# Optimization experiments

Hardware: AMD Instinct MI355X
Metric: run time of the kernel (lower is better)

## Reference

```python
import jax, jax.numpy as jnp
import numpy as np

PI = 3.14159265359  # TFPI constant from the source


def expected_relu(mu, sigma_sq):
    # Expected ReLU of N(mu, sigma_sq); exact ReLU where sigma_sq == 0 (observed).
    missing = sigma_sq != 0.0
    imputed = jnp.where(missing, sigma_sq, 1e-20)
    s = jnp.sqrt(imputed)
    w = mu / s
    vals = s * (jnp.exp(-0.5 * w * w) / jnp.sqrt(2.0 * PI)
                + 0.5 * w * (1.0 + jax.scipy.special.erf(w / jnp.sqrt(2.0))))
    return jnp.where(missing, vals, 0.5 * (mu + jnp.abs(mu)))


def setup_inputs() -> dict:
    key = jax.random.key(0)
    k0, k1, k2, k3, k4 = jax.random.split(key, 5)
    N, P, C, U = 65536, 256, 3, 512
    x = jax.random.normal(k0, (N, P), dtype=jnp.float32)
    nan_mask = jax.random.bernoulli(k1, 0.15, (N, P))
    x = jnp.where(nan_mask, jnp.nan, x)
    component_means = 0.5 * jax.random.normal(k2, (P, C), dtype=jnp.float32)
    component_vars = jax.random.uniform(k3, (P, C), dtype=jnp.float32, minval=0.5, maxval=1.5)
    component_logits = jnp.ones((C,), dtype=jnp.float32)
    kernel = jax.random.normal(k4, (P, U), dtype=jnp.float32) / np.float32(np.sqrt(P))
    bias = jnp.zeros((U,), dtype=jnp.float32)
    return {"x": x, "component_means": component_means, "component_vars": component_vars,
            "component_logits": component_logits, "kernel": kernel, "bias": bias}


def reference(x, component_means, component_vars, component_logits, kernel, bias):
    # x: [N, P] with NaNs; component_means/vars: [P, C]; logits: [C]; kernel: [P, U]; bias: [U]
    nan_mask = jnp.isnan(x)                       # [N, P]
    x_safe = jnp.where(nan_mask, 0.0, x)          # NaN-free copy (masked out below)
    mu_t = component_means.T                      # [C, P]
    var_t = component_vars.T                      # [C, P]
    # mvn_loglikelihood with NaN entries contributing 0
    q = -jnp.square(x_safe[:, None, :] - mu_t) / var_t / 2.0 - jnp.log(2.0 * PI * var_t) / 2.0  # [N, C, P]
    q = jnp.where(nan_mask[:, None, :], 0.0, q)
    loglik = jnp.sum(q, axis=-1)                  # [N, C]
    reweighted_p = jax.nn.softmax(component_logits + loglik, axis=-1)  # [N, C]
    # Impute missing entries with component means; variance nonzero only where missing
    means = jnp.where(nan_mask[..., None], component_means, x_safe[..., None])   # [N, P, C]
    variances = jnp.where(nan_mask[..., None], component_vars, 0.0)              # [N, P, C]
    layer_mean = jnp.einsum('npc,pu->cnu', means, kernel) + bias                 # [C, N, U]
    layer_var = jnp.einsum('npc,pu->cnu', variances, jnp.square(kernel))         # [C, N, U]
    layer_activation = expected_relu(layer_mean, layer_var)                      # [C, N, U]
    return jnp.einsum('nc,cnu->nu', reweighted_p, layer_activation)              # [N, U]
```

## Files before the change

### kernel.cpp

```cpp
#include <hip/hip_runtime.h>
#include <hip/hip_bf16.h>
#include <math.h>

#define N_ROWS 65536
#define P_DIM  256
#define C_DIM  3
#define U_DIM  512
#define NPLANES 7

#define BM 32
#define BU 64
#define NUT (U_DIM / BU)

typedef __attribute__((ext_vector_type(8))) short short8;
typedef __attribute__((ext_vector_type(4))) float f32x4;
typedef __attribute__((ext_vector_type(4))) float floatx4;
typedef __attribute__((ext_vector_type(4))) unsigned int uint4v;

static __device__ __forceinline__ unsigned short f2bf(float f) {
    unsigned int u = __builtin_bit_cast(unsigned int, f);
    u += 0x7FFFu + ((u >> 16) & 1u);
    return (unsigned short)(u >> 16);
}

static __device__ __forceinline__ float erl(float m, float v) {
    float r = __builtin_amdgcn_rsqf(fmaxf(v, 1e-20f));
    float w = m * r;
    float s = v * r;
    float g = __expf(w * w * -0.5f) * 0.3989422804014327f;
    float phi = __builtin_amdgcn_rcpf(1.0f + __expf(w * -1.702f));
    float val = s * g + m * phi;
    return (v > 0.0f) ? val : fmaxf(m, 0.0f);
}

__global__ __launch_bounds__(512) void prep_kernel(
    const float* __restrict__ cmeans, const float* __restrict__ cvars,
    const float* __restrict__ kern, unsigned short* __restrict__ Bf,
    float* __restrict__ qtab)
{
    int tid = blockIdx.x * 512 + threadIdx.x;
    const int TOTAL_B = NPLANES * U_DIM * P_DIM;
    if (tid < TOTAL_B) {
        int e    = tid & 7;
        int lane = (tid >> 3) & 63;
        int rest = tid >> 9;
        int pl   = rest % 7;
        int rk   = rest / 7;
        int ks   = rk & 7;
        int uw   = rk >> 3;
        int wc   = uw & 3;
        int ut   = uw >> 2;
        int u = ut * 64 + wc * 16 + (lane & 15);
        int k = ks * 32 + (lane >> 4) * 8 + e;
        float kv = kern[k * U_DIM + u];
        float val;
        if (pl == 0)      val = kv;
        else if (pl <= 3) val = cmeans[k * C_DIM + (pl - 1)] * kv;
        else              val = cvars[k * C_DIM + (pl - 4)] * (kv * kv);
        Bf[tid] = f2bf(val);
    } else if (tid - TOTAL_B < P_DIM) {
        int p = tid - TOTAL_B;
        float a[3], b[3], d[3];
#pragma unroll
        for (int c = 0; c < 3; ++c) {
            float m = cmeans[p * 3 + c];
            float v = cvars[p * 3 + c];
            float iv = 0.5f / v;
            a[c] = iv;
            b[c] = -2.0f * m * iv;
            d[c] = m * m * iv + 0.5f * logf(2.0f * 3.14159265359f * v);
        }
        float* q = qtab + p * 12;
        q[0] = a[0]; q[1] = a[1]; q[2]  = a[2]; q[3]  = 0.f;
        q[4] = b[0]; q[5] = b[1]; q[6]  = b[2]; q[7]  = 0.f;
        q[8] = d[0]; q[9] = d[1]; q[10] = d[2]; q[11] = 0.f;
    }
}

#define LOADBP(src, dst, nks) do {                                           \
    _Pragma("unroll")                                                         \
    for (int pl = 0; pl < NPLANES; ++pl)                                      \
        dst[pl] = *(const short8*)((src) + ((nks) * 7 + pl) * 512);           \
} while (0)

#define STEP(breg, ksi) do {                                                  \
    __builtin_amdgcn_s_setprio(1);                                            \
    _Pragma("unroll")                                                         \
    for (int r = 0; r < 2; ++r) {                                             \
        short8 a0 = *(const short8*)&xs[aBase + r * 4096 + (ksi) * 512];      \
        short8 a1 = *(const short8*)&mk[aBase + r * 4096 + (ksi) * 512];      \
        acc[0][r] = __builtin_amdgcn_mfma_f32_16x16x32_bf16(a0, breg[0], acc[0][r], 0, 0, 0); \
        _Pragma("unroll")                                                     \
        for (int pl = 1; pl < NPLANES; ++pl)                                  \
            acc[pl][r] = __builtin_amdgcn_mfma_f32_16x16x32_bf16(a1, breg[pl], acc[pl][r], 0, 0, 0); \
    }                                                                         \
    __builtin_amdgcn_s_setprio(0);                                            \
} while (0)

__global__ __launch_bounds__(256, 4) void main_kernel(
    const float* __restrict__ X, const unsigned short* __restrict__ Bf,
    const float* __restrict__ qtab, const float* __restrict__ logits,
    const float* __restrict__ bias, float* __restrict__ out)
{
    __shared__ unsigned short xs[BM * P_DIM];
    __shared__ unsigned short mk[BM * P_DIM];
    __shared__ float pws[BM][3];

    const int tid = threadIdx.x;
    const int n0 = blockIdx.x * BM;
    const int lane = tid & 63;
    const int wid  = tid >> 6;
    const int l15  = lane & 15;
    const int lk   = lane >> 4;

    {
        const int rowblk = wid >> 1;
        const int ksh    = (wid & 1) * 4;
        const float* Xb = X + (size_t)(n0 + rowblk * 16 + l15) * P_DIM + lk * 8;
        const int ebase = rowblk * 4096 + lk * 128 + l15 * 8;
#pragma unroll
        for (int j = 0; j < 4; ++j) {
            int ks = ksh + j;
            floatx4 v0 = *(const floatx4*)(Xb + ks * 32);
            floatx4 v1 = *(const floatx4*)(Xb + ks * 32 + 4);
            unsigned int wx[4], wm[4];
#pragma unroll
            for (int h = 0; h < 2; ++h) {
                floatx4 v = h ? v1 : v0;
#pragma unroll
                for (int e = 0; e < 2; ++e) {
                    float f0 = v[2 * e], f1 = v[2 * e + 1];
                    bool na0 = !(f0 == f0), na1 = !(f1 == f1);
                    unsigned int s0 = na0 ? 0u : (unsigned int)f2bf(f0);
                    unsigned int s1 = na1 ? 0u : (unsigned int)f2bf(f1);
                    unsigned int m0 = na0 ? 0x3F80u : 0u;
                    unsigned int m1 = na1 ? 0x3F80u : 0u;
                    wx[h * 2 + e] = s0 | (s1 << 16);
                    wm[h * 2 + e] = m0 | (m1 << 16);
                }
            }
            uint4v px = {wx[0], wx[1], wx[2], wx[3]};
            uint4v pm = {wm[0], wm[1], wm[2], wm[3]};
            *(uint4v*)&xs[ebase + ks * 512] = px;
            *(uint4v*)&mk[ebase + ks * 512] = pm;
        }
    }

    {
        int row = tid >> 3;
        int sub = tid & 7;
        const floatx4* xr = (const floatx4*)(X + (size_t)(n0 + row) * P_DIM);
        const floatx4* qt = (const floatx4*)qtab;
        float a0 = 0.f, a1 = 0.f, a2 = 0.f;
#pragma unroll
        for (int i = 0; i < 8; ++i) {
            floatx4 v = xr[sub * 8 + i];
#pragma unroll
            for (int e = 0; e < 4; ++e) {
                float x = v[e];
                int p = sub * 32 + i * 4 + e;
                bool valid = (x == x);
                float xv = valid ? x : 0.f;
                floatx4 qa = qt[p * 3 + 0];
                floatx4 qb = qt[p * 3 + 1];
                floatx4 qd = qt[p * 3 + 2];
                float q0 = fmaf(fmaf(qa[0], xv, qb[0]), xv, qd[0]);
                float q1 = fmaf(fmaf(qa[1], xv, qb[1]), xv, qd[1]);
                float q2 = fmaf(fmaf(qa[2], xv, qb[2]), xv, qd[2]);
                a0 += valid ? q0 : 0.f;
                a1 += valid ? q1 : 0.f;
                a2 += valid ? q2 : 0.f;
            }
        }
#pragma unroll
        for (int off = 1; off < 8; off <<= 1) {
            a0 += __shfl_xor(a0, off);
            a1 += __shfl_xor(a1, off);
            a2 += __shfl_xor(a2, off);
        }
        if (sub == 0) {
            float z0 = logits[0] - a0;
            float z1 = logits[1] - a1;
            float z2 = logits[2] - a2;
            float mx = fmaxf(z0, fmaxf(z1, z2));
            float e0 = __expf(z0 - mx), e1 = __expf(z1 - mx), e2 = __expf(z2 - mx);
            float inv = __builtin_amdgcn_rcpf(e0 + e1 + e2);
            pws[row][0] = e0 * inv;
            pws[row][1] = e1 * inv;
            pws[row][2] = e2 * inv;
        }
    }
    __syncthreads();

    const int wc = wid;
    const int aBase = lk * 128 + l15 * 8;
    const int phase = wc << 1;

    short8 bR[NPLANES];
    {
        const int utf = phase & (NUT - 1);
        const unsigned short* bpw0 = Bf + ((size_t)(utf * 4 + wc) * (8 * 7 * 512)) + (size_t)lane * 8;
        LOADBP(bpw0, bR, 0);
    }

#pragma unroll 1
    for (int ut0 = 0; ut0 < NUT; ++ut0) {
        const int ut  = (ut0 + phase) & (NUT - 1);
        const int utn = (ut0 + 1 + phase) & (NUT - 1);
        const unsigned short* bpw  = Bf + ((size_t)(ut  * 4 + wc) * (8 * 7 * 512)) + (size_t)lane * 8;
        const unsigned short* bpwn = Bf + ((size_t)(utn * 4 + wc) * (8 * 7 * 512)) + (size_t)lane * 8;

        f32x4 acc[NPLANES][2];
#pragma unroll
        for (int pl = 0; pl < NPLANES; ++pl)
#pragma unroll
            for (int r = 0; r < 2; ++r)
                acc[pl][r] = (f32x4){0.f, 0.f, 0.f, 0.f};

#pragma unroll 1
        for (int ks = 0; ks < 8; ++ks) {
            STEP(bR, ks);
            const unsigned short* nsrc = (ks == 7) ? bpwn : bpw;
            int nks = (ks + 1) & 7;
            LOADBP(nsrc, bR, nks);
            __builtin_amdgcn_sched_barrier(0);
        }

        const int ucol = ut * BU + wc * 16 + l15;
        const float bias_u = bias[ucol];
#pragma unroll
        for (int r = 0; r < 2; ++r) {
            int rloc = r * 16 + 4 * lk;
#pragma unroll
            for (int q = 0; q < 4; ++q) {
                int rl = rloc + q;
                float p0 = pws[rl][0], p1 = pws[rl][1], p2 = pws[rl][2];
                float y0 = acc[0][r][q] + bias_u;
                float res = p0 * erl(y0 + acc[1][r][q], acc[4][r][q])
                          + p1 * erl(y0 + acc[2][r][q], acc[5][r][q])
                          + p2 * erl(y0 + acc[3][r][q], acc[6][r][q]);
                out[(size_t)(n0 + rl) * U_DIM + ucol] = res;
            }
        }
    }
}

extern "C" void kernel_launch(void* const* d_in, const int* in_sizes, int n_in,
                              void* d_out, int out_size, void* d_ws, size_t ws_size,
                              hipStream_t stream)
{
    const float* X      = (const float*)d_in[0];
    const float* cmeans = (const float*)d_in[1];
    const float* cvars  = (const float*)d_in[2];
    const float* logits = (const float*)d_in[3];
    const float* kern   = (const float*)d_in[4];
    const float* bias   = (const float*)d_in[5];
    float* out = (float*)d_out;

    char* wsb = (char*)d_ws;
    unsigned short* Bf = (unsigned short*)wsb;
    float* qtab = (float*)(wsb + 1835008);

    hipLaunchKernelGGL(prep_kernel, dim3(1794), dim3(512), 0, stream,
                       cmeans, cvars, kern, Bf, qtab);
    hipLaunchKernelGGL(main_kernel, dim3(N_ROWS / BM), dim3(256), 0, stream,
                       X, Bf, qtab, logits, bias, out);
}
```

Measured before the change: 246.1 us.

## Simplify expected-ReLU math, stream B loads via pointer, stagger tile phase by block

```diff
diff --git a/kernel.cpp b/kernel.cpp
--- a/kernel.cpp
+++ b/kernel.cpp
@@ -27,9 +27,9 @@
     float r = __builtin_amdgcn_rsqf(fmaxf(v, 1e-20f));
     float w = m * r;
     float s = v * r;
-    float g = __expf(w * w * -0.5f) * 0.3989422804014327f;
-    float phi = __builtin_amdgcn_rcpf(1.0f + __expf(w * -1.702f));
-    float val = s * g + m * phi;
+    float e = __expf(w * -1.702f);
+    float t = __builtin_amdgcn_rcpf(1.0f + e);
+    float val = fmaf(m, t, 1.702f * s * t * t * e);
     return (v > 0.0f) ? val : fmaxf(m, 0.0f);
 }
 
@@ -77,10 +77,16 @@
     }
 }
 
-#define LOADBP(src, dst, nks) do {                                           \
-    _Pragma("unroll")                                                         \
-    for (int pl = 0; pl < NPLANES; ++pl)                                      \
-        dst[pl] = *(const short8*)((src) + ((nks) * 7 + pl) * 512);           \
+#define LOADBP(base, dst) do {                                                \
+    const unsigned short* _b0 = (base);                                       \
+    const unsigned short* _b1 = (base) + 2048;                                \
+    dst[0] = *(const short8*)(_b0);                                           \
+    dst[1] = *(const short8*)(_b0 + 512);                                     \
+    dst[2] = *(const short8*)(_b0 + 1024);                                    \
+    dst[3] = *(const short8*)(_b0 + 1536);                                    \
+    dst[4] = *(const short8*)(_b1);                                           \
+    dst[5] = *(const short8*)(_b1 + 512);                                     \
+    dst[6] = *(const short8*)(_b1 + 1024);                                    \
 } while (0)
 
 #define STEP(breg, ksi) do {                                                  \
@@ -194,20 +200,21 @@
 
     const int wc = wid;
     const int aBase = lk * 128 + l15 * 8;
-    const int phase = wc << 1;
+    const int phase = (int)(((unsigned)(wc + blockIdx.x) & 3u) << 1);
 
     short8 bR[NPLANES];
+    const unsigned short* nextp;
     {
         const int utf = phase & (NUT - 1);
         const unsigned short* bpw0 = Bf + ((size_t)(utf * 4 + wc) * (8 * 7 * 512)) + (size_t)lane * 8;
-        LOADBP(bpw0, bR, 0);
+        LOADBP(bpw0, bR);
+        nextp = bpw0 + 3584;
     }
 
 #pragma unroll 1
     for (int ut0 = 0; ut0 < NUT; ++ut0) {
         const int ut  = (ut0 + phase) & (NUT - 1);
         const int utn = (ut0 + 1 + phase) & (NUT - 1);
-        const unsigned short* bpw  = Bf + ((size_t)(ut  * 4 + wc) * (8 * 7 * 512)) + (size_t)lane * 8;
         const unsigned short* bpwn = Bf + ((size_t)(utn * 4 + wc) * (8 * 7 * 512)) + (size_t)lane * 8;
 
         f32x4 acc[NPLANES][2];
@@ -220,9 +227,8 @@
 #pragma unroll 1
         for (int ks = 0; ks < 8; ++ks) {
             STEP(bR, ks);
-            const unsigned short* nsrc = (ks == 7) ? bpwn : bpw;
-            int nks = (ks + 1) & 7;
-            LOADBP(nsrc, bR, nks);
+            LOADBP(nextp, bR);
+            nextp = (ks == 6) ? bpwn : (nextp + 3584);
             __builtin_amdgcn_sched_barrier(0);
         }
 
```

Measured after the change: 237.6 us, median of 3. 3.4% less time.
